# Optimization experiments

Hardware: AMD Instinct MI355X
Metric: run time of the kernel (lower is better)

## Reference

```python
import jax, jax.numpy as jnp
import numpy as np

SEQ_LEN = 512; PATCH = 16; STRIDE = 8; D_MODEL = 768; N_HEAD = 12; N_LAYERS = 6
POOL = 1000; TOP_K = 4; PRED_LEN = 96; TREND_W = 24; SEAS = 24
PATCH_NUM = (SEQ_LEN - PATCH) // STRIDE + 2  # 64, incl. the replication-padded patch
B = 64; M = 7


def _ln(x, g, b, eps=1e-5):
    mu = jnp.mean(x, axis=-1, keepdims=True)
    v = jnp.var(x, axis=-1, keepdims=True)
    return (x - mu) * jax.lax.rsqrt(v + eps) * g + b


def _decompose(x):
    # x: [N, L]. pandas: rolling(TREND_W, center=True).mean() + bfill/ffill,
    # then seasonal = groupby(index % SEAS).transform('mean') of detrended.
    N, L = x.shape
    w = TREND_W
    right = (w - 1) // 2          # pandas centered window: [i - (w-1-right), i + right]
    left = w - 1 - right
    cs = jnp.concatenate([jnp.zeros((N, 1), x.dtype), jnp.cumsum(x, axis=1)], axis=1)
    valid = (cs[:, w:] - cs[:, :-w]) / w                      # [N, L-w+1]
    trend = jnp.concatenate([jnp.repeat(valid[:, :1], left, axis=1), valid,
                             jnp.repeat(valid[:, -1:], right, axis=1)], axis=1)
    det = x - trend
    ids = jnp.arange(L) % SEAS
    onehot = jax.nn.one_hot(ids, SEAS, dtype=x.dtype)         # [L, S]
    gmean = (det @ onehot) / jnp.sum(onehot, axis=0)          # [N, S]
    seasonal = gmean[:, ids]
    resid = x - trend - seasonal
    return jnp.stack([trend, seasonal, resid], axis=1)        # [N, 3, L]


def _gpt2(h, wpe, layer_params, lnf_g, lnf_b):
    Bh, T, D = h.shape
    h = h + wpe[:T]
    mask = jnp.tril(jnp.ones((T, T), bool))
    hd = D // N_HEAD

    def block(h, p):
        ln1g, ln1b, qkvw, qkvb, aw, ab, ln2g, ln2b, fcw, fcb, pw, pb = p
        a = _ln(h, ln1g, ln1b)
        qkv = a @ qkvw + qkvb
        q, k, v = jnp.split(qkv, 3, axis=-1)
        sh = lambda t: t.reshape(Bh, T, N_HEAD, hd).transpose(0, 2, 1, 3)
        q, k, v = sh(q), sh(k), sh(v)
        s = jnp.einsum('bhqd,bhkd->bhqk', q, k) / jnp.sqrt(jnp.asarray(hd, h.dtype))
        s = jnp.where(mask, s, jnp.asarray(-1e9, h.dtype))
        att = jax.nn.softmax(s, axis=-1)
        o = jnp.einsum('bhqk,bhkd->bhqd', att, v).transpose(0, 2, 1, 3).reshape(Bh, T, D)
        h = h + o @ aw + ab
        m = _ln(h, ln2g, ln2b)
        h = h + jax.nn.gelu(m @ fcw + fcb, approximate=True) @ pw + pb
        return h, None

    h, _ = jax.lax.scan(block, h, layer_params)
    return _ln(h, lnf_g, lnf_b)


def setup_inputs() -> dict:
    key = jax.random.key(0)
    ks = jax.random.split(key, 10)
    D = D_MODEL; F = 4 * D
    f32 = jnp.float32
    return dict(
        x=jax.random.normal(ks[0], (B, SEQ_LEN, M), f32),
        itr=1,
        in_w=jax.random.normal(ks[1], (3 * PATCH, D), f32) * 0.02,
        in_b=jnp.zeros((D,), f32),
        prompt_key=jax.random.uniform(ks[2], (POOL, D), f32, -1.0, 1.0),
        wpe=jax.random.normal(ks[3], (1024, D), f32) * 0.02,
        ln1_g=jnp.ones((N_LAYERS, D), f32), ln1_b=jnp.zeros((N_LAYERS, D), f32),
        qkv_w=jax.random.normal(ks[4], (N_LAYERS, D, 3 * D), f32) * 0.02,
        qkv_b=jnp.zeros((N_LAYERS, 3 * D), f32),
        aproj_w=jax.random.normal(ks[5], (N_LAYERS, D, D), f32) * 0.02,
        aproj_b=jnp.zeros((N_LAYERS, D), f32),
        ln2_g=jnp.ones((N_LAYERS, D), f32), ln2_b=jnp.zeros((N_LAYERS, D), f32),
        fc_w=jax.random.normal(ks[6], (N_LAYERS, D, F), f32) * 0.02,
        fc_b=jnp.zeros((N_LAYERS, F), f32),
        mproj_w=jax.random.normal(ks[7], (N_LAYERS, F, D), f32) * 0.02,
        mproj_b=jnp.zeros((N_LAYERS, D), f32),
        lnf_g=jnp.ones((D,), f32), lnf_b=jnp.zeros((D,), f32),
        out_w=jax.random.normal(ks[8], ((D // 3) * (PATCH_NUM + TOP_K), PRED_LEN), f32) * 0.02,
        out_b=jnp.zeros((PRED_LEN,), f32),
    )


def reference(x, itr, in_w, in_b, prompt_key, wpe, ln1_g, ln1_b, qkv_w, qkv_b,
              aproj_w, aproj_b, ln2_g, ln2_b, fc_w, fc_b, mproj_w, mproj_b,
              lnf_g, lnf_b, out_w, out_b):
    B_, L, M_ = x.shape
    means = jax.lax.stop_gradient(jnp.mean(x, axis=1, keepdims=True))     # detached
    xc = x - means
    stdev = jax.lax.stop_gradient(jnp.sqrt(jnp.var(xc, axis=1, keepdims=True) + 1e-5))
    xn = xc / stdev
    xr = jnp.transpose(xn, (0, 2, 1)).reshape(B_ * M_, L)                  # 'b l m -> (b m) l'
    dec = jax.lax.stop_gradient(_decompose(xr))                            # torch detaches via numpy round-trip
    # ReplicationPad1d((0, STRIDE)) then unfold(size=PATCH, step=STRIDE)
    xpad = jnp.concatenate([dec, jnp.repeat(dec[:, :, -1:], STRIDE, axis=2)], axis=2)
    starts = jnp.arange(PATCH_NUM) * STRIDE
    patches = xpad[:, :, starts[:, None] + jnp.arange(PATCH)[None, :]]     # [BM, 3, N, P]
    tok = jnp.transpose(patches, (0, 2, 1, 3)).reshape(B_ * M_, PATCH_NUM, 3 * PATCH)
    emb = tok @ in_w + in_b                                                # [BM, N, D]
    # prompt-pool retrieval (L2P-style, length=1, prompts = normalized keys)
    l2n = lambda t: t * jax.lax.rsqrt(jnp.maximum(jnp.sum(t * t, -1, keepdims=True), 1e-12))
    key_n = l2n(prompt_key)                                                # [POOL, D]
    xq = l2n(jnp.mean(emb, axis=1))                                        # [BM, D]
    sim = xq @ key_n.T                                                     # [BM, POOL]
    _, idx = jax.lax.top_k(sim, TOP_K)
    bp = key_n[idx]                                                        # [BM, K, D]
    reduce_sim = jnp.sum(bp * xq[:, None, :]) / emb.shape[0]
    prompted = jnp.concatenate([bp, emb], axis=1)                          # [BM, K+N, D]
    layer_params = (ln1_g, ln1_b, qkv_w, qkv_b, aproj_w, aproj_b,
                    ln2_g, ln2_b, fc_w, fc_b, mproj_w, mproj_b)
    h = _gpt2(prompted, wpe, layer_params, lnf_g, lnf_b)                   # [BM, K+N, D]
    o = h.reshape(B_ * M_ * 3, -1) @ out_w + out_b                         # [BM*3, PRED_LEN]
    o = o.reshape(B_, M_, 3, PRED_LEN).sum(axis=2)                         # [B, M, H]
    out = jnp.transpose(o, (0, 2, 1)) * stdev + means                      # [B, H, M]
    return out, reduce_sim
```

## Files before the change

kernel.cpp:

```cpp
#include <hip/hip_runtime.h>
#include <math.h>

#define NTOK 30464
#define NEMB 28672
typedef unsigned short ushort;
typedef __attribute__((ext_vector_type(8))) __bf16 bf16x8_t;
typedef __attribute__((ext_vector_type(4))) float f32x4_t;

#if defined(__has_builtin)
#if __has_builtin(__builtin_amdgcn_global_load_lds)
#define HAS_GLL 1
#endif
#endif

__device__ __forceinline__ ushort f2bf(float f) {
  unsigned int u = __float_as_uint(f);
  u += 0x7fffu + ((u >> 16) & 1u);
  return (ushort)(u >> 16);
}
__device__ __forceinline__ float bf2f(ushort u) {
  return __uint_as_float(((unsigned int)u) << 16);
}

#ifdef HAS_GLL
__device__ __forceinline__ void gll16(const ushort* g, ushort* l) {
  __builtin_amdgcn_global_load_lds(
      (const __attribute__((address_space(1))) unsigned int*)g,
      (__attribute__((address_space(3))) unsigned int*)l, 16, 0, 0);
}
#endif

__device__ __forceinline__ float block_reduce_sum(float v, float* scratch) {
  __syncthreads();
  #pragma unroll
  for (int o = 32; o; o >>= 1) v += __shfl_xor(v, o, 64);
  int wid = threadIdx.x >> 6, lane = threadIdx.x & 63;
  if (lane == 0) scratch[wid] = v;
  __syncthreads();
  if (threadIdx.x == 0) {
    float s = 0.f;
    int nw = (blockDim.x + 63) >> 6;
    for (int i = 0; i < nw; i++) s += scratch[i];
    scratch[0] = s;
  }
  __syncthreads();
  return scratch[0];
}

__device__ __forceinline__ float gelu_f(float x) {
  float z2 = 1.5957691216057308f * (x + 0.044715f * x * x * x);
  return x / (1.0f + __expf(-z2));
}

__global__ __launch_bounds__(256) void revin_kernel(const float* __restrict__ x,
    float* __restrict__ xr, float* __restrict__ means, float* __restrict__ stdev) {
  int bm = blockIdx.x;
  int b = bm / 7, m = bm % 7;
  int tid = threadIdx.x;
  __shared__ float red[8];
  float v0 = x[(size_t)b * 3584 + (size_t)tid * 7 + m];
  float v1 = x[(size_t)b * 3584 + (size_t)(tid + 256) * 7 + m];
  float s  = block_reduce_sum(v0 + v1, red);
  float ss = block_reduce_sum(v0 * v0 + v1 * v1, red);
  float mean = s * (1.0f / 512.0f);
  float var  = ss * (1.0f / 512.0f) - mean * mean;
  float sd = sqrtf(var + 1e-5f);
  if (tid == 0) { means[bm] = mean; stdev[bm] = sd; }
  float inv = 1.0f / sd;
  xr[(size_t)bm * 512 + tid]       = (v0 - mean) * inv;
  xr[(size_t)bm * 512 + tid + 256] = (v1 - mean) * inv;
}

__global__ __launch_bounds__(256) void decompose_kernel(const float* __restrict__ xr,
    float* __restrict__ dec) {
  int n = blockIdx.x, tid = threadIdx.x;
  __shared__ float xv[512];
  __shared__ float tr[512];
  __shared__ float sumS[24];
  for (int l = tid; l < 512; l += 256) xv[l] = xr[(size_t)n * 512 + l];
  if (tid < 24) sumS[tid] = 0.f;
  __syncthreads();
  for (int l = tid; l < 512; l += 256) {
    int t0 = l - 12; t0 = t0 < 0 ? 0 : (t0 > 488 ? 488 : t0);
    float s = 0.f;
    #pragma unroll
    for (int j = 0; j < 24; j++) s += xv[t0 + j];
    float t = s * (1.0f / 24.0f);
    tr[l] = t;
    atomicAdd(&sumS[l % 24], xv[l] - t);
  }
  __syncthreads();
  if (tid < 24) sumS[tid] *= (tid < 8) ? (1.0f / 22.0f) : (1.0f / 21.0f);
  __syncthreads();
  float* dp = dec + (size_t)n * 1536;
  for (int l = tid; l < 512; l += 256) {
    float t = tr[l], se = sumS[l % 24];
    dp[l] = t;
    dp[512 + l] = se;
    dp[1024 + l] = xv[l] - t - se;
  }
}

__global__ __launch_bounds__(256) void embed_kernel(const float* __restrict__ dec,
    const float* __restrict__ in_w, const float* __restrict__ in_b, float* __restrict__ h) {
  int np = blockIdx.x;
  int n = np >> 6, p = np & 63;
  int tid = threadIdx.x;
  __shared__ float tok[48];
  if (tid < 48) {
    int c = tid >> 4, j = tid & 15;
    int l = p * 8 + j; if (l > 511) l = 511;
    tok[tid] = dec[(size_t)n * 1536 + (size_t)c * 512 + l];
  }
  __syncthreads();
  float* outp = h + ((size_t)n * 68 + 4 + p) * 768;
  #pragma unroll
  for (int i = 0; i < 3; i++) {
    int d = tid + i * 256;
    float acc = in_b[d];
    #pragma unroll
    for (int k = 0; k < 48; k++) acc += tok[k] * in_w[(size_t)k * 768 + d];
    outp[d] = acc;
  }
}

__global__ __launch_bounds__(256) void keyn_kernel(const float* __restrict__ pkey,
    float* __restrict__ keyn, double* __restrict__ kinv) {
  int k = blockIdx.x, tid = threadIdx.x;
  __shared__ double redd[4];
  float v[3];
  double ss = 0.0;
  #pragma unroll
  for (int i = 0; i < 3; i++) {
    v[i] = pkey[(size_t)k * 768 + tid + i * 256];
    ss += (double)v[i] * (double)v[i];
  }
  #pragma unroll
  for (int o = 32; o; o >>= 1) ss += __shfl_xor(ss, o, 64);
  int wid = tid >> 6, lane = tid & 63;
  if (lane == 0) redd[wid] = ss;
  __syncthreads();
  if (tid == 0) redd[0] = redd[0] + redd[1] + redd[2] + redd[3];
  __syncthreads();
  ss = redd[0];
  double inv = 1.0 / sqrt(ss > 1e-12 ? ss : 1e-12);
  #pragma unroll
  for (int i = 0; i < 3; i++)
    keyn[(size_t)k * 768 + tid + i * 256] = (float)((double)v[i] * inv);
  if (tid == 0) kinv[k] = inv;
}

__global__ __launch_bounds__(256) void xq_kernel(const float* __restrict__ h,
    float* __restrict__ xq) {
  int n = blockIdx.x, tid = threadIdx.x;
  __shared__ float red[8];
  float vals[3];
  float ssl = 0.f;
  #pragma unroll
  for (int i = 0; i < 3; i++) {
    int d = tid + i * 256;
    const float* p = h + ((size_t)n * 68 + 4) * 768 + d;
    float s = 0.f;
    for (int pc = 0; pc < 64; pc++) s += p[(size_t)pc * 768];
    s *= (1.0f / 64.0f);
    vals[i] = s; ssl += s * s;
  }
  float ss = block_reduce_sum(ssl, red);
  float inv = rsqrtf(fmaxf(ss, 1e-12f));
  #pragma unroll
  for (int i = 0; i < 3; i++)
    xq[(size_t)n * 768 + tid + i * 256] = vals[i] * inv;
}

__global__ void zero_kernel(float* p) {
  if (threadIdx.x == 0 && blockIdx.x == 0) p[0] = 0.f;
}

__global__ __launch_bounds__(256) void simtopk_kernel(
    const float* __restrict__ xq, const float* __restrict__ pkey,
    const double* __restrict__ kinv, const float* __restrict__ keyn,
    const float* __restrict__ wpe, float* __restrict__ h, float* __restrict__ rs_out) {
  int n = blockIdx.x, tid = threadIdx.x;
  __shared__ __align__(16) float xqv[768];
  __shared__ double simd_s[1000];
  __shared__ int idxs[4];
  __shared__ double redv[4];
  __shared__ int redi[4];
  __shared__ float red2[8];
  #pragma unroll
  for (int i = 0; i < 3; i++) xqv[tid + i * 256] = xq[(size_t)n * 768 + tid + i * 256];
  __syncthreads();
  int lane = tid & 63, wid = tid >> 6;
  for (int k4 = wid * 4; k4 < 1000; k4 += 16) {
    double a[4] = {0.0, 0.0, 0.0, 0.0};
    #pragma unroll
    for (int i = 0; i < 12; i++) {
      int d = lane + 64 * i;
      double xv = (double)xqv[d];
      #pragma unroll
      for (int t = 0; t < 4; t++)
        a[t] += (double)pkey[(size_t)(k4 + t) * 768 + d] * xv;
    }
    #pragma unroll
    for (int t = 0; t < 4; t++)
      #pragma unroll
      for (int o = 32; o; o >>= 1) a[t] += __shfl_xor(a[t], o, 64);
    if (lane == 0) {
      #pragma unroll
      for (int t = 0; t < 4; t++) simd_s[k4 + t] = a[t] * kinv[k4 + t];
    }
  }
  __syncthreads();
  for (int r = 0; r < 4; r++) {
    double bv = -1e300; int bi = 0x7fffffff;
    for (int k = tid; k < 1000; k += 256) {
      double v = simd_s[k];
      if (v > bv || (v == bv && k < bi)) { bv = v; bi = k; }
    }
    #pragma unroll
    for (int off = 32; off; off >>= 1) {
      double ov = __shfl_xor(bv, off, 64);
      int oi = __shfl_xor(bi, off, 64);
      if (ov > bv || (ov == bv && oi < bi)) { bv = ov; bi = oi; }
    }
    if (lane == 0) { redv[wid] = bv; redi[wid] = bi; }
    __syncthreads();
    if (tid == 0) {
      double fv = redv[0]; int fi = redi[0];
      for (int w = 1; w < 4; w++)
        if (redv[w] > fv || (redv[w] == fv && redi[w] < fi)) { fv = redv[w]; fi = redi[w]; }
      idxs[r] = fi; simd_s[fi] = -1e300;
    }
    __syncthreads();
  }
  float part = 0.f;
  for (int r = 0; r < 4; r++) {
    int ki = idxs[r];
    const float* kp = keyn + (size_t)ki * 768;
    const float* wp = wpe + (size_t)r * 768;
    float* hp = h + ((size_t)n * 68 + r) * 768;
    #pragma unroll
    for (int i = 0; i < 3; i++) {
      int d = tid + i * 256;
      float kv = kp[d];
      hp[d] = kv + wp[d];
      part += kv * xqv[d];
    }
  }
  part = block_reduce_sum(part, red2);
  if (tid == 0) atomicAdd(rs_out, part * (1.0f / 448.0f));
}

__global__ __launch_bounds__(256) void addwpe_kernel(const float* __restrict__ wpe,
    float* __restrict__ h) {
  int np = blockIdx.x;
  int n = np >> 6, p = np & 63;
  int tid = threadIdx.x;
  const float* wp = wpe + (size_t)(4 + p) * 768;
  float* hp = h + ((size_t)n * 68 + 4 + p) * 768;
  #pragma unroll
  for (int i = 0; i < 3; i++) { int d = tid + i * 256; hp[d] += wp[d]; }
}

__global__ __launch_bounds__(256) void ln_kernel(const float* __restrict__ src,
    ushort* __restrict__ dst, const float* __restrict__ g, const float* __restrict__ b) {
  size_t row = blockIdx.x;
  const float* xp = src + row * 768;
  ushort* yp = dst + row * 768;
  int tid = threadIdx.x;
  float v0 = xp[tid], v1 = xp[tid + 256], v2 = xp[tid + 512];
  __shared__ float red[8];
  float s  = block_reduce_sum(v0 + v1 + v2, red);
  float ss = block_reduce_sum(v0 * v0 + v1 * v1 + v2 * v2, red);
  float mean = s * (1.0f / 768.0f);
  float var  = ss * (1.0f / 768.0f) - mean * mean;
  float rs = rsqrtf(var + 1e-5f);
  yp[tid]       = f2bf((v0 - mean) * rs * g[tid]       + b[tid]);
  yp[tid + 256] = f2bf((v1 - mean) * rs * g[tid + 256] + b[tid + 256]);
  yp[tid + 512] = f2bf((v2 - mean) * rs * g[tid + 512] + b[tid + 512]);
}

__global__ __launch_bounds__(256) void tcast_kernel(const float* __restrict__ W,
    ushort* __restrict__ WT, int K, int N) {
  __shared__ ushort t[32][33];
  int n0 = blockIdx.x * 32, k0 = blockIdx.y * 32;
  int tx = threadIdx.x & 31, ty = threadIdx.x >> 5;
  #pragma unroll
  for (int i = 0; i < 4; i++) {
    int kk = ty + i * 8;
    t[kk][tx] = f2bf(W[(size_t)(k0 + kk) * N + n0 + tx]);
  }
  __syncthreads();
  #pragma unroll
  for (int i = 0; i < 4; i++) {
    int nn = ty + i * 8;
    WT[(size_t)(n0 + nn) * K + k0 + tx] = t[tx][nn];
  }
}

__global__ __launch_bounds__(256) void mfma_gemm(const ushort* __restrict__ A,
    const ushort* __restrict__ WT, const float* __restrict__ bias, void* __restrict__ Cp,
    int M, int N, int K, int mode) {
  __shared__ ushort As[128 * 32];
  __shared__ ushort Bs[128 * 32];
  const int tid = threadIdx.x;
  const int row0 = blockIdx.y * 128, col0 = blockIdx.x * 128;
  const int w = tid >> 6, lane = tid & 63;
  const int wm = w >> 1, wn = w & 1;
  const int lm = lane & 15, quad = lane >> 4;
  const int srow = w * 16 + (lane >> 2);
  const int scol = (lane & 3) * 8;
  const ushort* agp0 = A  + (size_t)(row0 + srow)      * K + scol;
  const ushort* agp1 = A  + (size_t)(row0 + 64 + srow) * K + scol;
  const ushort* bgp0 = WT + (size_t)(col0 + srow)      * K + scol;
  const ushort* bgp1 = WT + (size_t)(col0 + 64 + srow) * K + scol;
  ushort* al0 = &As[w * 512];
  ushort* al1 = &As[2048 + w * 512];
  ushort* bl0 = &Bs[w * 512];
  ushort* bl1 = &Bs[2048 + w * 512];
  f32x4_t acc[4][4];
  #pragma unroll
  for (int mi = 0; mi < 4; mi++)
    #pragma unroll
    for (int ni = 0; ni < 4; ni++) acc[mi][ni] = (f32x4_t)(0.0f);

  for (int kb = 0; kb < K; kb += 32) {
    __syncthreads();
#ifdef HAS_GLL
    gll16(agp0 + kb, al0);
    gll16(agp1 + kb, al1);
    gll16(bgp0 + kb, bl0);
    gll16(bgp1 + kb, bl1);
#else
    {
      uint4 va0 = *(const uint4*)(agp0 + kb);
      uint4 va1 = *(const uint4*)(agp1 + kb);
      uint4 vb0 = *(const uint4*)(bgp0 + kb);
      uint4 vb1 = *(const uint4*)(bgp1 + kb);
      *(uint4*)&al0[lane * 8] = va0;
      *(uint4*)&al1[lane * 8] = va1;
      *(uint4*)&bl0[lane * 8] = vb0;
      *(uint4*)&bl1[lane * 8] = vb1;
    }
#endif
    __syncthreads();
    bf16x8_t af[4], bfr[4];
    #pragma unroll
    for (int mi = 0; mi < 4; mi++)
      af[mi] = *(const bf16x8_t*)&As[(wm * 64 + mi * 16 + lm) * 32 + quad * 8];
    #pragma unroll
    for (int ni = 0; ni < 4; ni++)
      bfr[ni] = *(const bf16x8_t*)&Bs[(wn * 64 + ni * 16 + lm) * 32 + quad * 8];
    #pragma unroll
    for (int mi = 0; mi < 4; mi++)
      #pragma unroll
      for (int ni = 0; ni < 4; ni++)
        acc[mi][ni] = __builtin_amdgcn_mfma_f32_16x16x32_bf16(af[mi], bfr[ni], acc[mi][ni], 0, 0, 0);
  }
  #pragma unroll
  for (int mi = 0; mi < 4; mi++) {
    #pragma unroll
    for (int ni = 0; ni < 4; ni++) {
      int gcol = col0 + wn * 64 + ni * 16 + lm;
      float bz = bias[gcol];
      #pragma unroll
      for (int r = 0; r < 4; r++) {
        int grow = row0 + wm * 64 + mi * 16 + quad * 4 + r;
        float v = acc[mi][ni][r] + bz;
        if (mode == 0)      ((ushort*)Cp)[(size_t)grow * N + gcol] = f2bf(v);
        else if (mode == 1) ((ushort*)Cp)[(size_t)grow * N + gcol] = f2bf(gelu_f(v));
        else { float* c = (float*)Cp + (size_t)grow * N + gcol; *c += v; }
      }
    }
  }
}

__global__ __launch_bounds__(256) void attn_kernel(const ushort* __restrict__ qkvc,
    ushort* __restrict__ obase) {
  __shared__ __align__(16) ushort qk[2 * 80 * 64];
  __shared__ __align__(16) ushort vt[64][96];
  __shared__ __align__(16) float  sS[68][80];
  ushort* qs = qk;
  ushort* ks = qk + 80 * 64;
  ushort (*P)[96] = (ushort(*)[96])qk;

  int nh = blockIdx.x;
  int nl = nh / 12, hh = nh % 12;
  int tid = threadIdx.x;
  const int w = tid >> 6, lane = tid & 63;
  const int lm = lane & 15, quad = lane >> 4;
  const ushort* base = qkvc + (size_t)nl * 68 * 2304 + hh * 64;

  for (int idx = tid; idx < 68 * 64; idx += 256) {
    int t = idx >> 6, d = idx & 63;
    const ushort* rp = base + (size_t)t * 2304 + d;
    qs[t * 64 + d] = rp[0];
    ks[t * 64 + d] = rp[768];
    vt[d][t] = rp[1536];
  }
  for (int idx = tid; idx < 64 * 28; idx += 256) {
    int d = idx / 28, t = 68 + idx % 28;
    vt[d][t] = 0;
  }
  __syncthreads();

  for (int t5 = w; t5 < 25; t5 += 4) {
    int mi = t5 / 5, ni = t5 % 5;
    bf16x8_t a0 = *(const bf16x8_t*)&qs[(mi * 16 + lm) * 64 + quad * 8];
    bf16x8_t a1 = *(const bf16x8_t*)&qs[(mi * 16 + lm) * 64 + 32 + quad * 8];
    bf16x8_t b0 = *(const bf16x8_t*)&ks[(ni * 16 + lm) * 64 + quad * 8];
    bf16x8_t b1 = *(const bf16x8_t*)&ks[(ni * 16 + lm) * 64 + 32 + quad * 8];
    f32x4_t acc = (f32x4_t)(0.0f);
    acc = __builtin_amdgcn_mfma_f32_16x16x32_bf16(a0, b0, acc, 0, 0, 0);
    acc = __builtin_amdgcn_mfma_f32_16x16x32_bf16(a1, b1, acc, 0, 0, 0);
    int col = ni * 16 + lm;
    #pragma unroll
    for (int r = 0; r < 4; r++) {
      int row = mi * 16 + quad * 4 + r;
      if (row < 68) {
        float sv = (col > row || col >= 68) ? -1e9f : acc[r] * 0.125f;
        sS[row][col] = sv;
      }
    }
  }
  __syncthreads();

  if (tid < 68) {
    int r = tid;
    float mx = -1e30f;
    for (int c = 0; c < 80; c++) mx = fmaxf(mx, sS[r][c]);
    float sum = 0.f;
    for (int c = 0; c < 80; c++) { float e = __expf(sS[r][c] - mx); sS[r][c] = e; sum += e; }
    float inv = 1.0f / sum;
    for (int c = 0; c < 80; c++) P[r][c] = f2bf(sS[r][c] * inv);
    #pragma unroll
    for (int c = 80; c < 96; c++) P[r][c] = 0;
  } else if (tid < 80) {
    for (int c = 0; c < 96; c++) P[tid][c] = 0;
  }
  __syncthreads();

  for (int t5 = w; t5 < 20; t5 += 4) {
    int mi = t5 % 5, ni = t5 / 5;
    f32x4_t acc = (f32x4_t)(0.0f);
    #pragma unroll
    for (int kk = 0; kk < 3; kk++) {
      bf16x8_t a = *(const bf16x8_t*)&P[mi * 16 + lm][kk * 32 + quad * 8];
      bf16x8_t b = *(const bf16x8_t*)&vt[ni * 16 + lm][kk * 32 + quad * 8];
      acc = __builtin_amdgcn_mfma_f32_16x16x32_bf16(a, b, acc, 0, 0, 0);
    }
    int col = ni * 16 + lm;
    #pragma unroll
    for (int r = 0; r < 4; r++) {
      int row = mi * 16 + quad * 4 + r;
      if (row < 68)
        obase[((size_t)nl * 68 + row) * 768 + hh * 64 + col] = f2bf(acc[r]);
    }
  }
}

__global__ __launch_bounds__(256) void initof_kernel(const float* __restrict__ ob,
    float* __restrict__ of) {
  int i = blockIdx.x * 256 + threadIdx.x;
  of[i] = ob[i % 96];
}

__global__ __launch_bounds__(256) void splitk_kernel(const ushort* __restrict__ A,
    const ushort* __restrict__ WT, float* __restrict__ of) {
  __shared__ ushort As[64][40];
  __shared__ ushort Ws[96][40];
  int row0 = blockIdx.x * 64;
  int k0 = blockIdx.y * 1024;
  int tid = threadIdx.x;
  int tx = tid & 15, ty = tid >> 4;
  float acc[4][6] = {};
  for (int kb = k0; kb < k0 + 1024; kb += 32) {
    __syncthreads();
    {
      int m = tid >> 2, seg = (tid & 3) * 8;
      uint4 v = *(const uint4*)(A + (size_t)(row0 + m) * 17408 + kb + seg);
      *(uint4*)&As[m][seg] = v;
    }
    for (int idx = tid; idx < 384; idx += 256) {
      int n = idx >> 2, seg = (idx & 3) * 8;
      uint4 v = *(const uint4*)(WT + (size_t)n * 17408 + kb + seg);
      *(uint4*)&Ws[n][seg] = v;
    }
    __syncthreads();
    for (int k = 0; k < 32; k++) {
      float av[4], wv[6];
      #pragma unroll
      for (int i = 0; i < 4; i++) av[i] = bf2f(As[ty * 4 + i][k]);
      #pragma unroll
      for (int j = 0; j < 6; j++) wv[j] = bf2f(Ws[tx * 6 + j][k]);
      #pragma unroll
      for (int i = 0; i < 4; i++)
        #pragma unroll
        for (int j = 0; j < 6; j++) acc[i][j] += av[i] * wv[j];
    }
  }
  #pragma unroll
  for (int i = 0; i < 4; i++)
    #pragma unroll
    for (int j = 0; j < 6; j++)
      atomicAdd(&of[(size_t)(row0 + ty * 4 + i) * 96 + tx * 6 + j], acc[i][j]);
}

__global__ void combine_kernel(const float* __restrict__ of, const float* __restrict__ stdev,
    const float* __restrict__ means, float* __restrict__ out) {
  int bm = blockIdx.x;
  int b = bm / 7, m = bm % 7;
  int j = threadIdx.x;
  if (j < 96) {
    float s = of[(size_t)(bm * 3 + 0) * 96 + j]
            + of[(size_t)(bm * 3 + 1) * 96 + j]
            + of[(size_t)(bm * 3 + 2) * 96 + j];
    out[(size_t)b * 672 + (size_t)j * 7 + m] = s * stdev[bm] + means[bm];
  }
}

extern "C" void kernel_launch(void* const* d_in, const int* in_sizes, int n_in,
                              void* d_out, int out_size, void* d_ws, size_t ws_size,
                              hipStream_t stream) {
  (void)in_sizes; (void)n_in; (void)out_size;
  const float* x     = (const float*)d_in[0];
  const float* in_w  = (const float*)d_in[2];
  const float* in_b  = (const float*)d_in[3];
  const float* pkey  = (const float*)d_in[4];
  const float* wpe   = (const float*)d_in[5];
  const float* ln1_g = (const float*)d_in[6];
  const float* ln1_b = (const float*)d_in[7];
  const float* qkv_w = (const float*)d_in[8];
  const float* qkv_b = (const float*)d_in[9];
  const float* aw    = (const float*)d_in[10];
  const float* ab    = (const float*)d_in[11];
  const float* ln2_g = (const float*)d_in[12];
  const float* ln2_b = (const float*)d_in[13];
  const float* fc_w  = (const float*)d_in[14];
  const float* fc_b  = (const float*)d_in[15];
  const float* mp_w  = (const float*)d_in[16];
  const float* mp_b  = (const float*)d_in[17];
  const float* lnf_g = (const float*)d_in[18];
  const float* lnf_b = (const float*)d_in[19];
  const float* out_w = (const float*)d_in[20];
  const float* out_b = (const float*)d_in[21];
  float* out = (float*)d_out;
  float* ws  = (float*)d_ws;

  float* means = ws;
  float* stdev = ws + 512;
  float* xr    = ws + 1024;
  float* dec   = xr + 229376;
  float* keyn  = dec + 688128;
  double* kinv = (double*)(keyn + 768000);
  float* xq    = keyn + 768000 + 2048;
  float* of    = xq + 344064;
  float* h     = of + 129024;
  ushort* abuf16 = (ushort*)(h + 23396352);
  ushort* w16    = abuf16 + 23396352;
  ushort* scr16  = w16 + 7077888;
  ushort* owT16  = scr16;

  ushort* wqT  = w16;
  ushort* waT  = wqT + 2304 * 768;
  ushort* wfcT = waT + 768 * 768;
  ushort* wmpT = wfcT + 3072 * 768;

  size_t scr_bytes = ws_size - (size_t)((char*)scr16 - (char*)ws);
  long cap_qg = (long)(scr_bytes / (17ull * 128 * 2304 * 2));
  if (cap_qg > 14) cap_qg = 14;
  if (cap_qg < 1) cap_qg = 1;
  int nch_q = (int)((14 + cap_qg - 1) / cap_qg);
  int gpc = (14 + nch_q - 1) / nch_q;
  long cap_ft = (long)(scr_bytes / (128ull * 3072 * 2));
  if (cap_ft > 238) cap_ft = 238;
  if (cap_ft < 1) cap_ft = 1;
  int nch_f = (int)((238 + cap_ft - 1) / cap_ft);
  int tpc = (238 + nch_f - 1) / nch_f;

  revin_kernel<<<448, 256, 0, stream>>>(x, xr, means, stdev);
  decompose_kernel<<<448, 256, 0, stream>>>(xr, dec);
  embed_kernel<<<NEMB, 256, 0, stream>>>(dec, in_w, in_b, h);
  keyn_kernel<<<1000, 256, 0, stream>>>(pkey, keyn, kinv);
  xq_kernel<<<448, 256, 0, stream>>>(h, xq);
  zero_kernel<<<1, 64, 0, stream>>>(out + 43008);
  simtopk_kernel<<<448, 256, 0, stream>>>(xq, pkey, kinv, keyn, wpe, h, out + 43008);
  addwpe_kernel<<<NEMB, 256, 0, stream>>>(wpe, h);

  for (int l = 0; l < 6; l++) {
    tcast_kernel<<<dim3(72, 24), 256, 0, stream>>>(qkv_w + (size_t)l * 768 * 2304, wqT, 768, 2304);
    tcast_kernel<<<dim3(24, 24), 256, 0, stream>>>(aw    + (size_t)l * 768 * 768,  waT, 768, 768);
    tcast_kernel<<<dim3(96, 24), 256, 0, stream>>>(fc_w  + (size_t)l * 768 * 3072, wfcT, 768, 3072);
    tcast_kernel<<<dim3(24, 96), 256, 0, stream>>>(mp_w  + (size_t)l * 3072 * 768, wmpT, 3072, 768);

    ln_kernel<<<NTOK, 256, 0, stream>>>(h, abuf16, ln1_g + l * 768, ln1_b + l * 768);
    for (int g0 = 0; g0 < 14; ) {
      int g = (gpc < 14 - g0) ? gpc : (14 - g0);
      int tiles = g * 17, rows = g * 2176, series = g * 32;
      ushort* Ain = abuf16 + (size_t)g0 * 2176 * 768;
      mfma_gemm<<<dim3(18, tiles), 256, 0, stream>>>(
          Ain, wqT, qkv_b + l * 2304, scr16, rows, 2304, 768, 0);
      attn_kernel<<<series * 12, 256, 0, stream>>>(scr16, Ain);
      g0 += g;
    }
    mfma_gemm<<<dim3(6, 238), 256, 0, stream>>>(
        abuf16, waT, ab + l * 768, h, NTOK, 768, 768, 2);
    ln_kernel<<<NTOK, 256, 0, stream>>>(h, abuf16, ln2_g + l * 768, ln2_b + l * 768);
    for (int t0 = 0; t0 < 238; ) {
      int t = (tpc < 238 - t0) ? tpc : (238 - t0);
      mfma_gemm<<<dim3(24, t), 256, 0, stream>>>(
          abuf16 + (size_t)t0 * 128 * 768, wfcT, fc_b + l * 3072, scr16,
          t * 128, 3072, 768, 1);
      mfma_gemm<<<dim3(6, t), 256, 0, stream>>>(
          scr16, wmpT, mp_b + l * 768, h + (size_t)t0 * 128 * 768,
          t * 128, 768, 3072, 2);
      t0 += t;
    }
  }
  ln_kernel<<<NTOK, 256, 0, stream>>>(h, abuf16, lnf_g, lnf_b);
  tcast_kernel<<<dim3(3, 544), 256, 0, stream>>>(out_w, owT16, 17408, 96);
  initof_kernel<<<504, 256, 0, stream>>>(out_b, of);
  splitk_kernel<<<dim3(21, 17), 256, 0, stream>>>(abuf16, owT16, of);
  combine_kernel<<<448, 96, 0, stream>>>(of, stdev, means, out);
}
```

Before: 7.484 ms.

## Split prompt similarity and top-k into separate kernels with wider grid

The fused similarity+top-k kernel is split in two. A new sim kernel spreads the 1000 pool keys over 8 blocks per series, giving 3584 blocks instead of 448, and uses float4 loads with a per-lane contiguous slice of each key. The similarities go to a global scratch buffer that reuses the xr region. A separate top-k kernel then reads them back. This trades an extra launch and a global round trip for much more parallelism and better memory coalescing in the fp64 dot products. It also changes the fp64 summation order, which could alter top-k tie-breaking in rare cases.

```diff
diff --git a/kernel.cpp b/kernel.cpp
--- a/kernel.cpp
+++ b/kernel.cpp
@@ -176,10 +176,59 @@
   if (threadIdx.x == 0 && blockIdx.x == 0) p[0] = 0.f;
 }
 
-__global__ __launch_bounds__(256) void simtopk_kernel(
+__global__ __launch_bounds__(256) void sim_kernel(
     const float* __restrict__ xq, const float* __restrict__ pkey,
-    const double* __restrict__ kinv, const float* __restrict__ keyn,
-    const float* __restrict__ wpe, float* __restrict__ h, float* __restrict__ rs_out) {
+    const double* __restrict__ kinv, double* __restrict__ simd) {
+  int n = blockIdx.y;
+  int kbase = blockIdx.x * 128;
+  int tid = threadIdx.x;
+  __shared__ __align__(16) float xqv[768];
+  #pragma unroll
+  for (int i = 0; i < 3; i++) xqv[tid + i * 256] = xq[(size_t)n * 768 + tid + i * 256];
+  __syncthreads();
+  int lane = tid & 63, wid = tid >> 6;
+  double xd[12];
+  #pragma unroll
+  for (int i = 0; i < 12; i++) xd[i] = (double)xqv[lane * 12 + i];
+
+  for (int k4 = kbase + wid * 4; k4 < kbase + 128; k4 += 16) {
+    int kt[4];
+    #pragma unroll
+    for (int t = 0; t < 4; t++) { int k = k4 + t; kt[t] = k < 1000 ? k : 999; }
+    float4 v[4][3];
+    #pragma unroll
+    for (int t = 0; t < 4; t++)
+      #pragma unroll
+      for (int j = 0; j < 3; j++)
+        v[t][j] = *(const float4*)(pkey + (size_t)kt[t] * 768 + lane * 12 + j * 4);
+    double a[4] = {0.0, 0.0, 0.0, 0.0};
+    #pragma unroll
+    for (int t = 0; t < 4; t++)
+      #pragma unroll
+      for (int j = 0; j < 3; j++) {
+        a[t] += (double)v[t][j].x * xd[4 * j + 0];
+        a[t] += (double)v[t][j].y * xd[4 * j + 1];
+        a[t] += (double)v[t][j].z * xd[4 * j + 2];
+        a[t] += (double)v[t][j].w * xd[4 * j + 3];
+      }
+    #pragma unroll
+    for (int t = 0; t < 4; t++)
+      #pragma unroll
+      for (int o = 32; o; o >>= 1) a[t] += __shfl_xor(a[t], o, 64);
+    if (lane == 0) {
+      #pragma unroll
+      for (int t = 0; t < 4; t++) {
+        int k = k4 + t;
+        if (k < 1000) simd[(size_t)n * 1000 + k] = a[t] * kinv[k];
+      }
+    }
+  }
+}
+
+__global__ __launch_bounds__(256) void topk_kernel(
+    const float* __restrict__ xq, const double* __restrict__ simd_g,
+    const float* __restrict__ keyn, const float* __restrict__ wpe,
+    float* __restrict__ h, float* __restrict__ rs_out) {
   int n = blockIdx.x, tid = threadIdx.x;
   __shared__ __align__(16) float xqv[768];
   __shared__ double simd_s[1000];
@@ -189,28 +238,9 @@
   __shared__ float red2[8];
   #pragma unroll
   for (int i = 0; i < 3; i++) xqv[tid + i * 256] = xq[(size_t)n * 768 + tid + i * 256];
+  for (int k = tid; k < 1000; k += 256) simd_s[k] = simd_g[(size_t)n * 1000 + k];
   __syncthreads();
   int lane = tid & 63, wid = tid >> 6;
-  for (int k4 = wid * 4; k4 < 1000; k4 += 16) {
-    double a[4] = {0.0, 0.0, 0.0, 0.0};
-    #pragma unroll
-    for (int i = 0; i < 12; i++) {
-      int d = lane + 64 * i;
-      double xv = (double)xqv[d];
-      #pragma unroll
-      for (int t = 0; t < 4; t++)
-        a[t] += (double)pkey[(size_t)(k4 + t) * 768 + d] * xv;
-    }
-    #pragma unroll
-    for (int t = 0; t < 4; t++)
-      #pragma unroll
-      for (int o = 32; o; o >>= 1) a[t] += __shfl_xor(a[t], o, 64);
-    if (lane == 0) {
-      #pragma unroll
-      for (int t = 0; t < 4; t++) simd_s[k4 + t] = a[t] * kinv[k4 + t];
-    }
-  }
-  __syncthreads();
   for (int r = 0; r < 4; r++) {
     double bv = -1e300; int bi = 0x7fffffff;
     for (int k = tid; k < 1000; k += 256) {
@@ -561,6 +591,8 @@
   ushort* scr16  = w16 + 7077888;
   ushort* owT16  = scr16;
 
+  double* simd = (double*)xr;
+
   ushort* wqT  = w16;
   ushort* waT  = wqT + 2304 * 768;
   ushort* wfcT = waT + 768 * 768;
@@ -584,7 +616,8 @@
   keyn_kernel<<<1000, 256, 0, stream>>>(pkey, keyn, kinv);
   xq_kernel<<<448, 256, 0, stream>>>(h, xq);
   zero_kernel<<<1, 64, 0, stream>>>(out + 43008);
-  simtopk_kernel<<<448, 256, 0, stream>>>(xq, pkey, kinv, keyn, wpe, h, out + 43008);
+  sim_kernel<<<dim3(8, 448), 256, 0, stream>>>(xq, pkey, kinv, simd);
+  topk_kernel<<<448, 256, 0, stream>>>(xq, simd, keyn, wpe, h, out + 43008);
   addwpe_kernel<<<NEMB, 256, 0, stream>>>(wpe, h);
 
   for (int l = 0; l < 6; l++) {
```

Result: faster. 6.829 ms (-8.8%).
